# Optimization experiments

Measured on AMD Instinct MI355X. Metric: run time of the kernel, lower is better.

## Reference

```python
import jax, jax.numpy as jnp
import numpy as np


def setup_inputs() -> dict:
    key = jax.random.key(0)
    kq, kk = jax.random.split(key)
    B, Q, K, D = 32, 512, 512, 1024
    queries = jax.random.normal(kq, (B, Q, D), dtype=jnp.float32)
    keys = jax.random.normal(kk, (B, K, D), dtype=jnp.float32)
    # ProbabilityConverter learned scalars (is_temperature=True, is_bias=True)
    temperature = jnp.ones((), dtype=jnp.float32)
    bias = jnp.zeros((), dtype=jnp.float32)
    return {"queries": queries, "keys": keys, "temperature": temperature, "bias": bias}


def reference(queries, keys, temperature, bias):
    # Dot scoring: (B, Q, D) x (B, K, D) -> (B, Q, K)
    logits = jnp.einsum("bqd,bkd->bqk", queries, keys)
    # keys.eq(0.0)[:, :, :1].transpose(1, 2): mask positions where first key feature == 0
    key_mask = (keys[:, :, 0] == 0.0)[:, None, :]  # (B, 1, K)
    neg_inf = jnp.array(-jnp.inf, dtype=logits.dtype)
    logits = jnp.where(key_mask, neg_inf, logits)
    # confidence = sigmoid((logsumexp(logits) + bias) * temperature)
    approx_max_logit = jax.nn.logsumexp(logits, axis=-1)  # (B, Q)
    confidence = jax.nn.sigmoid((approx_max_logit + bias) * temperature)
    attn = jax.nn.softmax(logits, axis=-1)  # (B, Q, K)
    return attn, confidence
```

## Files before the change

kernel.cpp:

```cpp
#include <hip/hip_runtime.h>
#include <math.h>
#include <stdint.h>


#define NB 32
#define NQ 512
#define NK 512
#define ND 1024
#define BK 32
#define NT (ND / BK)
#define BM1 64
#define BM5 64
#define ASTRIDE 520
#define TILE_BYTES 65536
#define WS_TILES ((size_t)NB * NT * TILE_BYTES)
#define WS_TOTAL (WS_TILES + (size_t)NB * NK * 4)

typedef __attribute__((ext_vector_type(8))) short short8;
typedef __attribute__((ext_vector_type(4))) float f32x4;

__device__ __forceinline__ void bf_split(float x, unsigned& hbits, float& lo) {
  unsigned u = __float_as_uint(x);
  unsigned r = u + 0x7fffu + ((u >> 16) & 1u);
  hbits = r & 0xffff0000u;
  lo = x - __uint_as_float(hbits);
}
__device__ __forceinline__ unsigned pack_rn(float x0, float x1) {
  unsigned u0 = __float_as_uint(x0), u1 = __float_as_uint(x1);
  unsigned r0 = u0 + 0x7fffu + ((u0 >> 16) & 1u);
  unsigned r1 = u1 + 0x7fffu + ((u1 >> 16) & 1u);
  return (r0 >> 16) | (r1 & 0xffff0000u);
}

__device__ __forceinline__ int lds_off_write(int r, int c4) {
  int slot = ((c4 >> 1) + (r >> 1)) & 3;
  return r * 32 + slot * 8 + (c4 & 1) * 4;
}
__device__ __forceinline__ int lds_off_read(int r, int quad) {
  int slot = (quad + (r >> 1)) & 3;
  return r * 32 + slot * 8;
}

__global__ __launch_bounds__(256)
void convert_k(const float* __restrict__ Kg, unsigned char* __restrict__ ws) {
  const int bx = blockIdx.x;
  const int batch = bx >> 5, kt = bx & 31;
  const float* src = Kg + (size_t)batch * NK * ND + kt * BK;
  unsigned short* hiB = (unsigned short*)(ws + (size_t)bx * TILE_BYTES);
  unsigned short* loB = hiB + 32768 / 2;
  float* maskB = (float*)(ws + WS_TILES) + batch * NK;

#pragma unroll
  for (int i = 0; i < 16; ++i) {
    int idx = threadIdx.x + 256 * i;
    int c = idx >> 3, c4 = idx & 7;
    float4 v = *(const float4*)(src + (size_t)c * ND + c4 * 4);
    unsigned h0, h1, h2, h3;
    float l0, l1, l2, l3;
    bf_split(v.x, h0, l0); bf_split(v.y, h1, l1);
    bf_split(v.z, h2, l2); bf_split(v.w, h3, l3);
    int off = c * 32 + c4 * 4;
    *(uint2*)(&hiB[off]) = make_uint2((h0 >> 16) | h1, (h2 >> 16) | h3);
    *(uint2*)(&loB[off]) = make_uint2(pack_rn(l0, l1), pack_rn(l2, l3));
    if (kt == 0 && c4 == 0) maskB[c] = v.x;
  }
}

#define MFMA_BF16 __builtin_amdgcn_mfma_f32_16x16x32_bf16

#define BODY5(KT, CURB, NXTB)                                                  \
  do {                                                                         \
    if ((KT) + 1 < NT) {                                                       \
      const unsigned char* tb = wsB + (size_t)((KT) + 1) * TILE_BYTES;         \
      _Pragma("unroll") for (int nt = 0; nt < 4; ++nt) {                       \
        NXTB[2 * nt]     = *(const float4*)(tb + nt * 1024 + boff);            \
        NXTB[2 * nt + 1] = *(const float4*)(tb + 32768 + nt * 1024 + boff);    \
      }                                                                        \
    }                                                                          \
    const int ktL = (KT) & 15;                                                 \
    short8 ahi[4], alo[4];                                                     \
    _Pragma("unroll") for (int mt = 0; mt < 4; ++mt) {                         \
      int off = (mt * 16 + ln15) * ASTRIDE + ktL * 32 + quad * 8;              \
      ahi[mt] = *(const short8*)(&sAhi[off]);                                  \
      alo[mt] = *(const short8*)(&sAlo[off]);                                  \
    }                                                                          \
    _Pragma("unroll") for (int nt = 0; nt < 4; ++nt) {                         \
      short8 bhi = *(const short8*)(&CURB[2 * nt]);                            \
      short8 blo = *(const short8*)(&CURB[2 * nt + 1]);                        \
      _Pragma("unroll") for (int mt = 0; mt < 4; ++mt) {                       \
        acc[mt][nt] = MFMA_BF16(ahi[mt], bhi, acc[mt][nt], 0, 0, 0);           \
        acc[mt][nt] = MFMA_BF16(ahi[mt], blo, acc[mt][nt], 0, 0, 0);           \
        acc[mt][nt] = MFMA_BF16(alo[mt], bhi, acc[mt][nt], 0, 0, 0);           \
      }                                                                        \
    }                                                                          \
  } while (0)

__global__ __launch_bounds__(512, 2)
void attn_fused_v5(const float* __restrict__ Qg,
                   const unsigned char* __restrict__ ws,
                   const float* __restrict__ Tp, const float* __restrict__ Bp,
                   float* __restrict__ attn, float* __restrict__ conf) {
  __shared__ __align__(16) unsigned short sAhi[BM5 * ASTRIDE];
  __shared__ __align__(16) unsigned short sAlo[BM5 * ASTRIDE];
  __shared__ __align__(16) float sRedA[BM5][8];
  __shared__ __align__(16) float sRedB[BM5][8];

  const int tid = threadIdx.x;
  const int g = blockIdx.x;
  const int batch = (g & 7) | (((g >> 3) & 3) << 3);
  const int q0 = (g >> 5) * BM5;
  const int ln = tid & 63, w = tid >> 6;
  const int ln15 = ln & 15, quad = ln >> 4;
  const int col0 = w * 64;

  const float* Qp = Qg + ((size_t)batch * NQ + q0) * ND;
  const unsigned char* wsB = ws + (size_t)batch * NT * TILE_BYTES;
  const float* maskB = (const float*)(ws + WS_TILES) + batch * NK;

  const int boff = (col0 << 6) + (ln15 << 6) + (quad << 4);

  f32x4 acc[4][4];
#pragma unroll
  for (int mt = 0; mt < 4; ++mt)
#pragma unroll
    for (int nt = 0; nt < 4; ++nt) acc[mt][nt] = (f32x4){0.f, 0.f, 0.f, 0.f};

  auto stage_half = [&](int h) {
#pragma unroll
    for (int i = 0; i < 16; ++i) {
      int idx = tid + 512 * i;
      int row = idx >> 7, kc4 = idx & 127;
      float4 v = *(const float4*)(Qp + (size_t)row * ND + h * 512 + kc4 * 4);
      unsigned h0, h1, h2, h3;
      float l0, l1, l2, l3;
      bf_split(v.x, h0, l0); bf_split(v.y, h1, l1);
      bf_split(v.z, h2, l2); bf_split(v.w, h3, l3);
      int off = row * ASTRIDE + kc4 * 4;
      *(uint2*)(&sAhi[off]) = make_uint2((h0 >> 16) | h1, (h2 >> 16) | h3);
      *(uint2*)(&sAlo[off]) = make_uint2(pack_rn(l0, l1), pack_rn(l2, l3));
    }
  };

  stage_half(0);
  float4 pbA[8], pbB[8];
#pragma unroll
  for (int nt = 0; nt < 4; ++nt) {
    pbA[2 * nt]     = *(const float4*)(wsB + nt * 1024 + boff);
    pbA[2 * nt + 1] = *(const float4*)(wsB + 32768 + nt * 1024 + boff);
  }
  __syncthreads();

#pragma unroll 1
  for (int kt = 0; kt < 16; kt += 2) {
    BODY5(kt, pbA, pbB);
    BODY5(kt + 1, pbB, pbA);
  }

  __syncthreads();
  stage_half(1);
  __syncthreads();

#pragma unroll 1
  for (int kt = 16; kt < 32; kt += 2) {
    BODY5(kt, pbA, pbB);
    BODY5(kt + 1, pbB, pbA);
  }

  const float NEGINF = -__builtin_inff();
  float rm[4][4];
#pragma unroll
  for (int mt = 0; mt < 4; ++mt)
#pragma unroll
    for (int rg = 0; rg < 4; ++rg) rm[mt][rg] = NEGINF;

#pragma unroll
  for (int nt = 0; nt < 4; ++nt) {
    int col = col0 + nt * 16 + ln15;
    bool msk = (maskB[col] == 0.0f);
#pragma unroll
    for (int mt = 0; mt < 4; ++mt)
#pragma unroll
      for (int rg = 0; rg < 4; ++rg) {
        float v = msk ? NEGINF : acc[mt][nt][rg];
        acc[mt][nt][rg] = v;
        rm[mt][rg] = fmaxf(rm[mt][rg], v);
      }
  }
#pragma unroll
  for (int mt = 0; mt < 4; ++mt)
#pragma unroll
    for (int rg = 0; rg < 4; ++rg) {
      float v = rm[mt][rg];
#pragma unroll
      for (int d = 1; d < 16; d <<= 1) v = fmaxf(v, __shfl_xor(v, d, 64));
      rm[mt][rg] = v;
    }
  if (ln15 == 0) {
#pragma unroll
    for (int mt = 0; mt < 4; ++mt)
#pragma unroll
      for (int rg = 0; rg < 4; ++rg)
        sRedA[mt * 16 + quad * 4 + rg][w] = rm[mt][rg];
  }
  __syncthreads();

  float gmax[4][4], gsum[4][4];
#pragma unroll
  for (int mt = 0; mt < 4; ++mt)
#pragma unroll
    for (int rg = 0; rg < 4; ++rg) {
      int row = mt * 16 + quad * 4 + rg;
      f32x4 p0 = *(const f32x4*)(&sRedA[row][0]);
      f32x4 p1 = *(const f32x4*)(&sRedA[row][4]);
      gmax[mt][rg] = fmaxf(fmaxf(fmaxf(p0[0], p0[1]), fmaxf(p0[2], p0[3])),
                           fmaxf(fmaxf(p1[0], p1[1]), fmaxf(p1[2], p1[3])));
      gsum[mt][rg] = 0.f;
    }

#pragma unroll
  for (int nt = 0; nt < 4; ++nt)
#pragma unroll
    for (int mt = 0; mt < 4; ++mt)
#pragma unroll
      for (int rg = 0; rg < 4; ++rg) {
        float e = __expf(acc[mt][nt][rg] - gmax[mt][rg]);
        acc[mt][nt][rg] = e;
        gsum[mt][rg] += e;
      }
#pragma unroll
  for (int mt = 0; mt < 4; ++mt)
#pragma unroll
    for (int rg = 0; rg < 4; ++rg) {
      float v = gsum[mt][rg];
#pragma unroll
      for (int d = 1; d < 16; d <<= 1) v += __shfl_xor(v, d, 64);
      gsum[mt][rg] = v;
    }
  if (ln15 == 0) {
#pragma unroll
    for (int mt = 0; mt < 4; ++mt)
#pragma unroll
      for (int rg = 0; rg < 4; ++rg)
        sRedB[mt * 16 + quad * 4 + rg][w] = gsum[mt][rg];
  }
  __syncthreads();
#pragma unroll
  for (int mt = 0; mt < 4; ++mt)
#pragma unroll
    for (int rg = 0; rg < 4; ++rg) {
      int row = mt * 16 + quad * 4 + rg;
      f32x4 p0 = *(const f32x4*)(&sRedB[row][0]);
      f32x4 p1 = *(const f32x4*)(&sRedB[row][4]);
      gsum[mt][rg] = (p0[0] + p0[1]) + (p0[2] + p0[3]) +
                     ((p1[0] + p1[1]) + (p1[2] + p1[3]));
    }

  float* outBase = attn + ((size_t)batch * NQ + q0) * NK;
#pragma unroll
  for (int mt = 0; mt < 4; ++mt)
#pragma unroll
    for (int rg = 0; rg < 4; ++rg) {
      int row = mt * 16 + quad * 4 + rg;
      float inv = 1.0f / gsum[mt][rg];
#pragma unroll
      for (int nt = 0; nt < 4; ++nt)
        outBase[(size_t)row * NK + col0 + nt * 16 + ln15] = acc[mt][nt][rg] * inv;
    }

  if (w == 0 && ln15 == 0) {
    float tv = Tp[0], bv = Bp[0];
#pragma unroll
    for (int mt = 0; mt < 4; ++mt)
#pragma unroll
      for (int rg = 0; rg < 4; ++rg) {
        int row = mt * 16 + quad * 4 + rg;
        float lse = gmax[mt][rg] + __logf(gsum[mt][rg]);
        float t = (lse + bv) * tv;
        conf[(size_t)batch * NQ + q0 + row] = 1.0f / (1.0f + __expf(-t));
      }
  }
}

__global__ __launch_bounds__(256, 1)
void attn_fused_v1(const float* __restrict__ Qg, const float* __restrict__ Kg,
                   const float* __restrict__ Tp, const float* __restrict__ Bp,
                   float* __restrict__ attn, float* __restrict__ conf) {
  __shared__ __align__(16) unsigned short sAhi[BM1 * BK];
  __shared__ __align__(16) unsigned short sAlo[BM1 * BK];
  __shared__ __align__(16) unsigned short sBhi[NK * BK];
  __shared__ __align__(16) unsigned short sBlo[NK * BK];
  __shared__ float sRedA[4][BM1];
  __shared__ float sRedB[4][BM1];

  const int tid = threadIdx.x;
  const int g = blockIdx.x;
  const int batch = (g & 7) | (((g >> 3) & 3) << 3);
  const int q0 = (g >> 5) * BM1;
  const int ln = tid & 63, w = tid >> 6;
  const int ln15 = ln & 15, quad = ln >> 4;
  const int wn0 = w * 128;

  const float* Qp = Qg + ((size_t)batch * NQ + q0) * ND;
  const float* Kp = Kg + (size_t)batch * NK * ND;

  f32x4 acc[4][8];
#pragma unroll
  for (int mt = 0; mt < 4; ++mt)
#pragma unroll
    for (int nt = 0; nt < 8; ++nt) acc[mt][nt] = (f32x4){0.f, 0.f, 0.f, 0.f};

  float4 pb[16], pa[2];
#pragma unroll
  for (int i = 0; i < 16; ++i) {
    int idx = tid + 256 * i, r = idx >> 3, c4 = idx & 7;
    pb[i] = *(const float4*)(Kp + (size_t)r * ND + c4 * 4);
  }
#pragma unroll
  for (int i = 0; i < 2; ++i) {
    int idx = tid + 256 * i, r = idx >> 3, c4 = idx & 7;
    pa[i] = *(const float4*)(Qp + (size_t)r * ND + c4 * 4);
  }

  for (int kt = 0; kt < NT; ++kt) {
    if (kt) __syncthreads();
#pragma unroll
    for (int i = 0; i < 2; ++i) {
      int idx = tid + 256 * i, r = idx >> 3, c4 = idx & 7;
      int off = lds_off_write(r, c4);
      unsigned h0, h1, h2, h3; float l0, l1, l2, l3;
      bf_split(pa[i].x, h0, l0); bf_split(pa[i].y, h1, l1);
      bf_split(pa[i].z, h2, l2); bf_split(pa[i].w, h3, l3);
      *(uint2*)(&sAhi[off]) = make_uint2((h0 >> 16) | h1, (h2 >> 16) | h3);
      *(uint2*)(&sAlo[off]) = make_uint2(pack_rn(l0, l1), pack_rn(l2, l3));
    }
#pragma unroll
    for (int i = 0; i < 16; ++i) {
      int idx = tid + 256 * i, r = idx >> 3, c4 = idx & 7;
      int off = lds_off_write(r, c4);
      unsigned h0, h1, h2, h3; float l0, l1, l2, l3;
      bf_split(pb[i].x, h0, l0); bf_split(pb[i].y, h1, l1);
      bf_split(pb[i].z, h2, l2); bf_split(pb[i].w, h3, l3);
      *(uint2*)(&sBhi[off]) = make_uint2((h0 >> 16) | h1, (h2 >> 16) | h3);
      *(uint2*)(&sBlo[off]) = make_uint2(pack_rn(l0, l1), pack_rn(l2, l3));
    }
    __syncthreads();

    if (kt < NT - 1) {
      const float* Kq = Kp + (kt + 1) * BK;
      const float* Qq = Qp + (kt + 1) * BK;
#pragma unroll
      for (int i = 0; i < 16; ++i) {
        int idx = tid + 256 * i, r = idx >> 3, c4 = idx & 7;
        pb[i] = *(const float4*)(Kq + (size_t)r * ND + c4 * 4);
      }
#pragma unroll
      for (int i = 0; i < 2; ++i) {
        int idx = tid + 256 * i, r = idx >> 3, c4 = idx & 7;
        pa[i] = *(const float4*)(Qq + (size_t)r * ND + c4 * 4);
      }
    }

    short8 ahi[4], alo[4];
#pragma unroll
    for (int mt = 0; mt < 4; ++mt) {
      int off = lds_off_read(mt * 16 + ln15, quad);
      ahi[mt] = *(const short8*)(&sAhi[off]);
      alo[mt] = *(const short8*)(&sAlo[off]);
    }
#pragma unroll
    for (int nt = 0; nt < 8; ++nt) {
      int off = lds_off_read(wn0 + nt * 16 + ln15, quad);
      short8 bhi = *(const short8*)(&sBhi[off]);
      short8 blo = *(const short8*)(&sBlo[off]);
#pragma unroll
      for (int mt = 0; mt < 4; ++mt) {
        acc[mt][nt] = MFMA_BF16(ahi[mt], bhi, acc[mt][nt], 0, 0, 0);
        acc[mt][nt] = MFMA_BF16(ahi[mt], blo, acc[mt][nt], 0, 0, 0);
        acc[mt][nt] = MFMA_BF16(alo[mt], bhi, acc[mt][nt], 0, 0, 0);
      }
    }
  }

  const float NEGINF = -__builtin_inff();
  float rm[4][4];
#pragma unroll
  for (int mt = 0; mt < 4; ++mt)
#pragma unroll
    for (int rg = 0; rg < 4; ++rg) rm[mt][rg] = NEGINF;
#pragma unroll
  for (int nt = 0; nt < 8; ++nt) {
    int col = wn0 + nt * 16 + ln15;
    bool msk = (Kp[(size_t)col * ND] == 0.0f);
#pragma unroll
    for (int mt = 0; mt < 4; ++mt)
#pragma unroll
      for (int rg = 0; rg < 4; ++rg) {
        float v = msk ? NEGINF : acc[mt][nt][rg];
        acc[mt][nt][rg] = v;
        rm[mt][rg] = fmaxf(rm[mt][rg], v);
      }
  }
#pragma unroll
  for (int mt = 0; mt < 4; ++mt)
#pragma unroll
    for (int rg = 0; rg < 4; ++rg) {
      float v = rm[mt][rg];
#pragma unroll
      for (int d = 1; d < 16; d <<= 1) v = fmaxf(v, __shfl_xor(v, d, 64));
      rm[mt][rg] = v;
    }
  if (ln15 == 0)
#pragma unroll
    for (int mt = 0; mt < 4; ++mt)
#pragma unroll
      for (int rg = 0; rg < 4; ++rg)
        sRedA[w][mt * 16 + quad * 4 + rg] = rm[mt][rg];
  __syncthreads();

  float gmax[4][4], gsum[4][4];
#pragma unroll
  for (int mt = 0; mt < 4; ++mt)
#pragma unroll
    for (int rg = 0; rg < 4; ++rg) {
      int row = mt * 16 + quad * 4 + rg;
      gmax[mt][rg] = fmaxf(fmaxf(sRedA[0][row], sRedA[1][row]),
                           fmaxf(sRedA[2][row], sRedA[3][row]));
      gsum[mt][rg] = 0.f;
    }
#pragma unroll
  for (int nt = 0; nt < 8; ++nt)
#pragma unroll
    for (int mt = 0; mt < 4; ++mt)
#pragma unroll
      for (int rg = 0; rg < 4; ++rg) {
        float e = __expf(acc[mt][nt][rg] - gmax[mt][rg]);
        acc[mt][nt][rg] = e;
        gsum[mt][rg] += e;
      }
#pragma unroll
  for (int mt = 0; mt < 4; ++mt)
#pragma unroll
    for (int rg = 0; rg < 4; ++rg) {
      float v = gsum[mt][rg];
#pragma unroll
      for (int d = 1; d < 16; d <<= 1) v += __shfl_xor(v, d, 64);
      gsum[mt][rg] = v;
    }
  if (ln15 == 0)
#pragma unroll
    for (int mt = 0; mt < 4; ++mt)
#pragma unroll
      for (int rg = 0; rg < 4; ++rg)
        sRedB[w][mt * 16 + quad * 4 + rg] = gsum[mt][rg];
  __syncthreads();
#pragma unroll
  for (int mt = 0; mt < 4; ++mt)
#pragma unroll
    for (int rg = 0; rg < 4; ++rg) {
      int row = mt * 16 + quad * 4 + rg;
      gsum[mt][rg] = sRedB[0][row] + sRedB[1][row] + sRedB[2][row] + sRedB[3][row];
    }

  float* outBase = attn + ((size_t)batch * NQ + q0) * NK;
#pragma unroll
  for (int mt = 0; mt < 4; ++mt)
#pragma unroll
    for (int rg = 0; rg < 4; ++rg) {
      int row = mt * 16 + quad * 4 + rg;
      float inv = 1.0f / gsum[mt][rg];
#pragma unroll
      for (int nt = 0; nt < 8; ++nt)
        outBase[(size_t)row * NK + wn0 + nt * 16 + ln15] = acc[mt][nt][rg] * inv;
    }
  if (w == 0 && ln15 == 0) {
    float tv = Tp[0], bv = Bp[0];
#pragma unroll
    for (int mt = 0; mt < 4; ++mt)
#pragma unroll
      for (int rg = 0; rg < 4; ++rg) {
        int row = mt * 16 + quad * 4 + rg;
        float lse = gmax[mt][rg] + __logf(gsum[mt][rg]);
        float t = (lse + bv) * tv;
        conf[(size_t)batch * NQ + q0 + row] = 1.0f / (1.0f + __expf(-t));
      }
  }
}

extern "C" void kernel_launch(void* const* d_in, const int* in_sizes, int n_in,
                              void* d_out, int out_size, void* d_ws, size_t ws_size,
                              hipStream_t stream) {
  const float* q = (const float*)d_in[0];
  const float* k = (const float*)d_in[1];
  const float* temp = (const float*)d_in[2];
  const float* bias = (const float*)d_in[3];
  float* attn = (float*)d_out;
  float* conf = attn + (size_t)NB * NQ * NK;

  if (ws_size >= WS_TOTAL) {
    hipLaunchKernelGGL(convert_k, dim3(NB * NT), dim3(256), 0, stream,
                       k, (unsigned char*)d_ws);
    hipLaunchKernelGGL(attn_fused_v5, dim3(NB * (NQ / BM5)), dim3(512), 0, stream,
                       q, (const unsigned char*)d_ws, temp, bias, attn, conf);
  } else {
    hipLaunchKernelGGL(attn_fused_v1, dim3(NB * (NQ / BM1)), dim3(256), 0, stream,
                       q, k, temp, bias, attn, conf);
  }
}
```

Baseline: 212.6 us.

## Split bf16x3 GEMM into two passes with separate hi/lo key planes

```diff
diff --git a/kernel.cpp b/kernel.cpp
--- a/kernel.cpp
+++ b/kernel.cpp
@@ -10,10 +10,13 @@
 #define BK 32
 #define NT (ND / BK)
 #define BM1 64
-#define BM5 64
-#define ASTRIDE 520
+#define BM6 64
+#define AS1 520
+#define AS2 1032
 #define TILE_BYTES 65536
-#define WS_TILES ((size_t)NB * NT * TILE_BYTES)
+#define PLANE_BYTES (NT * 32768)
+#define BATCH_WS (2 * PLANE_BYTES)
+#define WS_TILES ((size_t)NB * BATCH_WS)
 #define WS_TOTAL (WS_TILES + (size_t)NB * NK * 4)
 
 typedef __attribute__((ext_vector_type(8))) short short8;
@@ -31,6 +34,10 @@
   unsigned r1 = u1 + 0x7fffu + ((u1 >> 16) & 1u);
   return (r0 >> 16) | (r1 & 0xffff0000u);
 }
+__device__ __forceinline__ unsigned hi_rn(float x) {
+  unsigned u = __float_as_uint(x);
+  return (u + 0x7fffu + ((u >> 16) & 1u)) & 0xffff0000u;
+}
 
 __device__ __forceinline__ int lds_off_write(int r, int c4) {
   int slot = ((c4 >> 1) + (r >> 1)) & 3;
@@ -46,8 +53,9 @@
   const int bx = blockIdx.x;
   const int batch = bx >> 5, kt = bx & 31;
   const float* src = Kg + (size_t)batch * NK * ND + kt * BK;
-  unsigned short* hiB = (unsigned short*)(ws + (size_t)bx * TILE_BYTES);
-  unsigned short* loB = hiB + 32768 / 2;
+  unsigned short* hiB =
+      (unsigned short*)(ws + (size_t)batch * BATCH_WS + (size_t)kt * 32768);
+  unsigned short* loB = (unsigned short*)((unsigned char*)hiB + PLANE_BYTES);
   float* maskB = (float*)(ws + WS_TILES) + batch * NK;
 
 #pragma unroll
@@ -68,53 +76,71 @@
 
 #define MFMA_BF16 __builtin_amdgcn_mfma_f32_16x16x32_bf16
 
-#define BODY5(KT, CURB, NXTB)                                                  \
+#define BODY_P1(KT, CURB, NXTB)                                                \
   do {                                                                         \
     if ((KT) + 1 < NT) {                                                       \
-      const unsigned char* tb = wsB + (size_t)((KT) + 1) * TILE_BYTES;         \
-      _Pragma("unroll") for (int nt = 0; nt < 4; ++nt) {                       \
-        NXTB[2 * nt]     = *(const float4*)(tb + nt * 1024 + boff);            \
-        NXTB[2 * nt + 1] = *(const float4*)(tb + 32768 + nt * 1024 + boff);    \
-      }                                                                        \
+      const unsigned char* tb = wsHi + (size_t)((KT) + 1) * 32768;             \
+      _Pragma("unroll") for (int nt = 0; nt < 4; ++nt)                         \
+        NXTB[nt] = *(const f32x4*)(tb + nt * 1024 + boff);                     \
     }                                                                          \
     const int ktL = (KT) & 15;                                                 \
     short8 ahi[4], alo[4];                                                     \
     _Pragma("unroll") for (int mt = 0; mt < 4; ++mt) {                         \
-      int off = (mt * 16 + ln15) * ASTRIDE + ktL * 32 + quad * 8;              \
+      int off = (mt * 16 + ln15) * AS1 + ktL * 32 + quad * 8;                  \
       ahi[mt] = *(const short8*)(&sAhi[off]);                                  \
       alo[mt] = *(const short8*)(&sAlo[off]);                                  \
     }                                                                          \
     _Pragma("unroll") for (int nt = 0; nt < 4; ++nt) {                         \
-      short8 bhi = *(const short8*)(&CURB[2 * nt]);                            \
-      short8 blo = *(const short8*)(&CURB[2 * nt + 1]);                        \
+      short8 bhi = *(const short8*)(&CURB[nt]);                                \
       _Pragma("unroll") for (int mt = 0; mt < 4; ++mt) {                       \
         acc[mt][nt] = MFMA_BF16(ahi[mt], bhi, acc[mt][nt], 0, 0, 0);           \
-        acc[mt][nt] = MFMA_BF16(ahi[mt], blo, acc[mt][nt], 0, 0, 0);           \
         acc[mt][nt] = MFMA_BF16(alo[mt], bhi, acc[mt][nt], 0, 0, 0);           \
       }                                                                        \
     }                                                                          \
   } while (0)
 
+#define BODY_P2(KT, CURB, NXTB)                                                \
+  do {                                                                         \
+    if ((KT) + 1 < NT) {                                                       \
+      const unsigned char* tb = wsLo + (size_t)((KT) + 1) * 32768;             \
+      _Pragma("unroll") for (int nt = 0; nt < 4; ++nt)                         \
+        NXTB[nt] = *(const f32x4*)(tb + nt * 1024 + boff);                     \
+    }                                                                          \
+    short8 ahi2[4];                                                            \
+    _Pragma("unroll") for (int mt = 0; mt < 4; ++mt) {                         \
+      int off = (mt * 16 + ln15) * AS2 + (KT) * 32 + quad * 8;                 \
+      ahi2[mt] = *(const short8*)(&sA2[off]);                                  \
+    }                                                                          \
+    _Pragma("unroll") for (int nt = 0; nt < 4; ++nt) {                         \
+      short8 blo = *(const short8*)(&CURB[nt]);                                \
+      _Pragma("unroll") for (int mt = 0; mt < 4; ++mt)                         \
+        acc[mt][nt] = MFMA_BF16(ahi2[mt], blo, acc[mt][nt], 0, 0, 0);          \
+    }                                                                          \
+  } while (0)
+
 __global__ __launch_bounds__(512, 2)
-void attn_fused_v5(const float* __restrict__ Qg,
+void attn_fused_v6(const float* __restrict__ Qg,
                    const unsigned char* __restrict__ ws,
                    const float* __restrict__ Tp, const float* __restrict__ Bp,
                    float* __restrict__ attn, float* __restrict__ conf) {
-  __shared__ __align__(16) unsigned short sAhi[BM5 * ASTRIDE];
-  __shared__ __align__(16) unsigned short sAlo[BM5 * ASTRIDE];
-  __shared__ __align__(16) float sRedA[BM5][8];
-  __shared__ __align__(16) float sRedB[BM5][8];
+  __shared__ __align__(16) unsigned short sU[2 * BM6 * AS1];
+  __shared__ __align__(16) float sRedA[BM6][8];
+  __shared__ __align__(16) float sRedB[BM6][8];
+  unsigned short* sAhi = sU;
+  unsigned short* sAlo = sU + BM6 * AS1;
+  unsigned short* sA2 = sU;
 
   const int tid = threadIdx.x;
   const int g = blockIdx.x;
-  const int batch = (g & 7) | (((g >> 3) & 3) << 3);
-  const int q0 = (g >> 5) * BM5;
+  const int batch = g & 31;
+  const int q0 = (g >> 5) * BM6;
   const int ln = tid & 63, w = tid >> 6;
   const int ln15 = ln & 15, quad = ln >> 4;
   const int col0 = w * 64;
 
   const float* Qp = Qg + ((size_t)batch * NQ + q0) * ND;
-  const unsigned char* wsB = ws + (size_t)batch * NT * TILE_BYTES;
+  const unsigned char* wsHi = ws + (size_t)batch * BATCH_WS;
+  const unsigned char* wsLo = wsHi + PLANE_BYTES;
   const float* maskB = (const float*)(ws + WS_TILES) + batch * NK;
 
   const int boff = (col0 << 6) + (ln15 << 6) + (quad << 4);
@@ -125,45 +151,70 @@
 #pragma unroll
     for (int nt = 0; nt < 4; ++nt) acc[mt][nt] = (f32x4){0.f, 0.f, 0.f, 0.f};
 
-  auto stage_half = [&](int h) {
+  auto stage_p1 = [&](int h) {
 #pragma unroll
     for (int i = 0; i < 16; ++i) {
       int idx = tid + 512 * i;
       int row = idx >> 7, kc4 = idx & 127;
-      float4 v = *(const float4*)(Qp + (size_t)row * ND + h * 512 + kc4 * 4);
+      f32x4 v = __builtin_nontemporal_load(
+          (const f32x4*)(Qp + (size_t)row * ND + h * 512 + kc4 * 4));
       unsigned h0, h1, h2, h3;
       float l0, l1, l2, l3;
-      bf_split(v.x, h0, l0); bf_split(v.y, h1, l1);
-      bf_split(v.z, h2, l2); bf_split(v.w, h3, l3);
-      int off = row * ASTRIDE + kc4 * 4;
+      bf_split(v[0], h0, l0); bf_split(v[1], h1, l1);
+      bf_split(v[2], h2, l2); bf_split(v[3], h3, l3);
+      int off = row * AS1 + kc4 * 4;
       *(uint2*)(&sAhi[off]) = make_uint2((h0 >> 16) | h1, (h2 >> 16) | h3);
       *(uint2*)(&sAlo[off]) = make_uint2(pack_rn(l0, l1), pack_rn(l2, l3));
     }
   };
-
-  stage_half(0);
-  float4 pbA[8], pbB[8];
-#pragma unroll
-  for (int nt = 0; nt < 4; ++nt) {
-    pbA[2 * nt]     = *(const float4*)(wsB + nt * 1024 + boff);
-    pbA[2 * nt + 1] = *(const float4*)(wsB + 32768 + nt * 1024 + boff);
-  }
+  auto stage_p2 = [&]() {
+#pragma unroll
+    for (int i = 0; i < 32; ++i) {
+      int idx = tid + 512 * i;
+      int row = idx >> 8, kc4 = idx & 255;
+      f32x4 v = __builtin_nontemporal_load(
+          (const f32x4*)(Qp + (size_t)row * ND + kc4 * 4));
+      unsigned h0 = hi_rn(v[0]), h1 = hi_rn(v[1]);
+      unsigned h2 = hi_rn(v[2]), h3 = hi_rn(v[3]);
+      int off = row * AS2 + kc4 * 4;
+      *(uint2*)(&sA2[off]) = make_uint2((h0 >> 16) | h1, (h2 >> 16) | h3);
+    }
+  };
+
+  float4 pbA_[4], pbB_[4];
+  f32x4* pbA = (f32x4*)pbA_;
+  f32x4* pbB = (f32x4*)pbB_;
+
+  stage_p1(0);
+#pragma unroll
+  for (int nt = 0; nt < 4; ++nt)
+    pbA[nt] = *(const f32x4*)(wsHi + nt * 1024 + boff);
   __syncthreads();
 
 #pragma unroll 1
   for (int kt = 0; kt < 16; kt += 2) {
-    BODY5(kt, pbA, pbB);
-    BODY5(kt + 1, pbB, pbA);
-  }
-
-  __syncthreads();
-  stage_half(1);
-  __syncthreads();
-
+    BODY_P1(kt, pbA, pbB);
+    BODY_P1(kt + 1, pbB, pbA);
+  }
+  __syncthreads();
+  stage_p1(1);
+  __syncthreads();
 #pragma unroll 1
   for (int kt = 16; kt < 32; kt += 2) {
-    BODY5(kt, pbA, pbB);
-    BODY5(kt + 1, pbB, pbA);
+    BODY_P1(kt, pbA, pbB);
+    BODY_P1(kt + 1, pbB, pbA);
+  }
+
+  __syncthreads();
+#pragma unroll
+  for (int nt = 0; nt < 4; ++nt)
+    pbA[nt] = *(const f32x4*)(wsLo + nt * 1024 + boff);
+  stage_p2();
+  __syncthreads();
+#pragma unroll 1
+  for (int kt = 0; kt < 32; kt += 2) {
+    BODY_P2(kt, pbA, pbB);
+    BODY_P2(kt + 1, pbB, pbA);
   }
 
   const float NEGINF = -__builtin_inff();
@@ -264,7 +315,9 @@
       float inv = 1.0f / gsum[mt][rg];
 #pragma unroll
       for (int nt = 0; nt < 4; ++nt)
-        outBase[(size_t)row * NK + col0 + nt * 16 + ln15] = acc[mt][nt][rg] * inv;
+        __builtin_nontemporal_store(
+            acc[mt][nt][rg] * inv,
+            &outBase[(size_t)row * NK + col0 + nt * 16 + ln15]);
     }
 
   if (w == 0 && ln15 == 0) {
@@ -294,7 +347,7 @@
 
   const int tid = threadIdx.x;
   const int g = blockIdx.x;
-  const int batch = (g & 7) | (((g >> 3) & 3) << 3);
+  const int batch = g & 31;
   const int q0 = (g >> 5) * BM1;
   const int ln = tid & 63, w = tid >> 6;
   const int ln15 = ln & 15, quad = ln >> 4;
@@ -499,7 +552,7 @@
   if (ws_size >= WS_TOTAL) {
     hipLaunchKernelGGL(convert_k, dim3(NB * NT), dim3(256), 0, stream,
                        k, (unsigned char*)d_ws);
-    hipLaunchKernelGGL(attn_fused_v5, dim3(NB * (NQ / BM5)), dim3(512), 0, stream,
+    hipLaunchKernelGGL(attn_fused_v6, dim3(NB * (NQ / BM6)), dim3(512), 0, stream,
                        q, (const unsigned char*)d_ws, temp, bias, attn, conf);
   } else {
     hipLaunchKernelGGL(attn_fused_v1, dim3(NB * (NQ / BM1)), dim3(256), 0, stream,
```

Result: slower. 223.8 us (+5.3%).

## Double block width to 1024 threads with 16 waves each owning 32 key columns

Applied to the files above, without the earlier changes.

```diff
diff --git a/kernel.cpp b/kernel.cpp
--- a/kernel.cpp
+++ b/kernel.cpp
@@ -10,7 +10,7 @@
 #define BK 32
 #define NT (ND / BK)
 #define BM1 64
-#define BM5 64
+#define BM7 64
 #define ASTRIDE 520
 #define TILE_BYTES 65536
 #define WS_TILES ((size_t)NB * NT * TILE_BYTES)
@@ -68,14 +68,14 @@
 
 #define MFMA_BF16 __builtin_amdgcn_mfma_f32_16x16x32_bf16
 
-#define BODY5(KT, CURB, NXTB)                                                  \
+#define BODY7(KT, CURB, NXTB)                                                  \
   do {                                                                         \
     if ((KT) + 1 < NT) {                                                       \
       const unsigned char* tb = wsB + (size_t)((KT) + 1) * TILE_BYTES;         \
-      _Pragma("unroll") for (int nt = 0; nt < 4; ++nt) {                       \
-        NXTB[2 * nt]     = *(const float4*)(tb + nt * 1024 + boff);            \
-        NXTB[2 * nt + 1] = *(const float4*)(tb + 32768 + nt * 1024 + boff);    \
-      }                                                                        \
+      NXTB[0] = *(const f32x4*)(tb + boff);                                    \
+      NXTB[1] = *(const f32x4*)(tb + 1024 + boff);                             \
+      NXTB[2] = *(const f32x4*)(tb + 32768 + boff);                            \
+      NXTB[3] = *(const f32x4*)(tb + 32768 + 1024 + boff);                     \
     }                                                                          \
     const int ktL = (KT) & 15;                                                 \
     short8 ahi[4], alo[4];                                                     \
@@ -84,9 +84,9 @@
       ahi[mt] = *(const short8*)(&sAhi[off]);                                  \
       alo[mt] = *(const short8*)(&sAlo[off]);                                  \
     }                                                                          \
-    _Pragma("unroll") for (int nt = 0; nt < 4; ++nt) {                         \
-      short8 bhi = *(const short8*)(&CURB[2 * nt]);                            \
-      short8 blo = *(const short8*)(&CURB[2 * nt + 1]);                        \
+    _Pragma("unroll") for (int nt = 0; nt < 2; ++nt) {                         \
+      short8 bhi = *(const short8*)(&CURB[nt]);                                \
+      short8 blo = *(const short8*)(&CURB[2 + nt]);                            \
       _Pragma("unroll") for (int mt = 0; mt < 4; ++mt) {                       \
         acc[mt][nt] = MFMA_BF16(ahi[mt], bhi, acc[mt][nt], 0, 0, 0);           \
         acc[mt][nt] = MFMA_BF16(ahi[mt], blo, acc[mt][nt], 0, 0, 0);           \
@@ -95,23 +95,23 @@
     }                                                                          \
   } while (0)
 
-__global__ __launch_bounds__(512, 2)
-void attn_fused_v5(const float* __restrict__ Qg,
+__global__ __launch_bounds__(1024, 4)
+void attn_fused_v7(const float* __restrict__ Qg,
                    const unsigned char* __restrict__ ws,
                    const float* __restrict__ Tp, const float* __restrict__ Bp,
                    float* __restrict__ attn, float* __restrict__ conf) {
-  __shared__ __align__(16) unsigned short sAhi[BM5 * ASTRIDE];
-  __shared__ __align__(16) unsigned short sAlo[BM5 * ASTRIDE];
-  __shared__ __align__(16) float sRedA[BM5][8];
-  __shared__ __align__(16) float sRedB[BM5][8];
+  __shared__ __align__(16) unsigned short sAhi[BM7 * ASTRIDE];
+  __shared__ __align__(16) unsigned short sAlo[BM7 * ASTRIDE];
+  __shared__ __align__(16) float sRedA[BM7][16];
+  __shared__ __align__(16) float sRedB[BM7][16];
 
   const int tid = threadIdx.x;
   const int g = blockIdx.x;
-  const int batch = (g & 7) | (((g >> 3) & 3) << 3);
-  const int q0 = (g >> 5) * BM5;
+  const int batch = g & 31;
+  const int q0 = (g >> 5) * BM7;
   const int ln = tid & 63, w = tid >> 6;
   const int ln15 = ln & 15, quad = ln >> 4;
-  const int col0 = w * 64;
+  const int col0 = w * 32;
 
   const float* Qp = Qg + ((size_t)batch * NQ + q0) * ND;
   const unsigned char* wsB = ws + (size_t)batch * NT * TILE_BYTES;
@@ -119,41 +119,48 @@
 
   const int boff = (col0 << 6) + (ln15 << 6) + (quad << 4);
 
-  f32x4 acc[4][4];
-#pragma unroll
-  for (int mt = 0; mt < 4; ++mt)
-#pragma unroll
-    for (int nt = 0; nt < 4; ++nt) acc[mt][nt] = (f32x4){0.f, 0.f, 0.f, 0.f};
+  f32x4 acc[4][2];
+#pragma unroll
+  for (int mt = 0; mt < 4; ++mt)
+#pragma unroll
+    for (int nt = 0; nt < 2; ++nt) acc[mt][nt] = (f32x4){0.f, 0.f, 0.f, 0.f};
 
   auto stage_half = [&](int h) {
 #pragma unroll
-    for (int i = 0; i < 16; ++i) {
-      int idx = tid + 512 * i;
-      int row = idx >> 7, kc4 = idx & 127;
-      float4 v = *(const float4*)(Qp + (size_t)row * ND + h * 512 + kc4 * 4);
-      unsigned h0, h1, h2, h3;
-      float l0, l1, l2, l3;
-      bf_split(v.x, h0, l0); bf_split(v.y, h1, l1);
-      bf_split(v.z, h2, l2); bf_split(v.w, h3, l3);
-      int off = row * ASTRIDE + kc4 * 4;
-      *(uint2*)(&sAhi[off]) = make_uint2((h0 >> 16) | h1, (h2 >> 16) | h3);
-      *(uint2*)(&sAlo[off]) = make_uint2(pack_rn(l0, l1), pack_rn(l2, l3));
+    for (int i = 0; i < 4; ++i) {
+      int idx = tid + 1024 * i;
+      int row = idx >> 6, kc8 = idx & 63;
+      const float* p = Qp + (size_t)row * ND + h * 512 + kc8 * 8;
+      float4 va = *(const float4*)(p);
+      float4 vb = *(const float4*)(p + 4);
+      unsigned h0, h1, h2, h3, h4, h5, h6, h7;
+      float l0, l1, l2, l3, l4, l5, l6, l7;
+      bf_split(va.x, h0, l0); bf_split(va.y, h1, l1);
+      bf_split(va.z, h2, l2); bf_split(va.w, h3, l3);
+      bf_split(vb.x, h4, l4); bf_split(vb.y, h5, l5);
+      bf_split(vb.z, h6, l6); bf_split(vb.w, h7, l7);
+      int off = row * ASTRIDE + kc8 * 8;
+      *(uint4*)(&sAhi[off]) = make_uint4((h0 >> 16) | h1, (h2 >> 16) | h3,
+                                         (h4 >> 16) | h5, (h6 >> 16) | h7);
+      *(uint4*)(&sAlo[off]) = make_uint4(pack_rn(l0, l1), pack_rn(l2, l3),
+                                         pack_rn(l4, l5), pack_rn(l6, l7));
     }
   };
 
   stage_half(0);
-  float4 pbA[8], pbB[8];
-#pragma unroll
-  for (int nt = 0; nt < 4; ++nt) {
-    pbA[2 * nt]     = *(const float4*)(wsB + nt * 1024 + boff);
-    pbA[2 * nt + 1] = *(const float4*)(wsB + 32768 + nt * 1024 + boff);
-  }
+  float4 pbA_[4], pbB_[4];
+  f32x4* pbA = (f32x4*)pbA_;
+  f32x4* pbB = (f32x4*)pbB_;
+  pbA[0] = *(const f32x4*)(wsB + boff);
+  pbA[1] = *(const f32x4*)(wsB + 1024 + boff);
+  pbA[2] = *(const f32x4*)(wsB + 32768 + boff);
+  pbA[3] = *(const f32x4*)(wsB + 32768 + 1024 + boff);
   __syncthreads();
 
 #pragma unroll 1
   for (int kt = 0; kt < 16; kt += 2) {
-    BODY5(kt, pbA, pbB);
-    BODY5(kt + 1, pbB, pbA);
+    BODY7(kt, pbA, pbB);
+    BODY7(kt + 1, pbB, pbA);
   }
 
   __syncthreads();
@@ -162,8 +169,8 @@
 
 #pragma unroll 1
   for (int kt = 16; kt < 32; kt += 2) {
-    BODY5(kt, pbA, pbB);
-    BODY5(kt + 1, pbB, pbA);
+    BODY7(kt, pbA, pbB);
+    BODY7(kt + 1, pbB, pbA);
   }
 
   const float NEGINF = -__builtin_inff();
@@ -174,7 +181,7 @@
     for (int rg = 0; rg < 4; ++rg) rm[mt][rg] = NEGINF;
 
 #pragma unroll
-  for (int nt = 0; nt < 4; ++nt) {
+  for (int nt = 0; nt < 2; ++nt) {
     int col = col0 + nt * 16 + ln15;
     bool msk = (maskB[col] == 0.0f);
 #pragma unroll
@@ -212,13 +219,18 @@
       int row = mt * 16 + quad * 4 + rg;
       f32x4 p0 = *(const f32x4*)(&sRedA[row][0]);
       f32x4 p1 = *(const f32x4*)(&sRedA[row][4]);
-      gmax[mt][rg] = fmaxf(fmaxf(fmaxf(p0[0], p0[1]), fmaxf(p0[2], p0[3])),
-                           fmaxf(fmaxf(p1[0], p1[1]), fmaxf(p1[2], p1[3])));
+      f32x4 p2 = *(const f32x4*)(&sRedA[row][8]);
+      f32x4 p3 = *(const f32x4*)(&sRedA[row][12]);
+      float m01 = fmaxf(fmaxf(fmaxf(p0[0], p0[1]), fmaxf(p0[2], p0[3])),
+                        fmaxf(fmaxf(p1[0], p1[1]), fmaxf(p1[2], p1[3])));
+      float m23 = fmaxf(fmaxf(fmaxf(p2[0], p2[1]), fmaxf(p2[2], p2[3])),
+                        fmaxf(fmaxf(p3[0], p3[1]), fmaxf(p3[2], p3[3])));
+      gmax[mt][rg] = fmaxf(m01, m23);
       gsum[mt][rg] = 0.f;
     }
 
 #pragma unroll
-  for (int nt = 0; nt < 4; ++nt)
+  for (int nt = 0; nt < 2; ++nt)
 #pragma unroll
     for (int mt = 0; mt < 4; ++mt)
 #pragma unroll
@@ -251,8 +263,12 @@
       int row = mt * 16 + quad * 4 + rg;
       f32x4 p0 = *(const f32x4*)(&sRedB[row][0]);
       f32x4 p1 = *(const f32x4*)(&sRedB[row][4]);
-      gsum[mt][rg] = (p0[0] + p0[1]) + (p0[2] + p0[3]) +
-                     ((p1[0] + p1[1]) + (p1[2] + p1[3]));
+      f32x4 p2 = *(const f32x4*)(&sRedB[row][8]);
+      f32x4 p3 = *(const f32x4*)(&sRedB[row][12]);
+      gsum[mt][rg] = ((p0[0] + p0[1]) + (p0[2] + p0[3])) +
+                     ((p1[0] + p1[1]) + (p1[2] + p1[3])) +
+                     ((p2[0] + p2[1]) + (p2[2] + p2[3])) +
+                     ((p3[0] + p3[1]) + (p3[2] + p3[3]));
     }
 
   float* outBase = attn + ((size_t)batch * NQ + q0) * NK;
@@ -263,7 +279,7 @@
       int row = mt * 16 + quad * 4 + rg;
       float inv = 1.0f / gsum[mt][rg];
 #pragma unroll
-      for (int nt = 0; nt < 4; ++nt)
+      for (int nt = 0; nt < 2; ++nt)
         outBase[(size_t)row * NK + col0 + nt * 16 + ln15] = acc[mt][nt][rg] * inv;
     }
 
@@ -294,7 +310,7 @@
 
   const int tid = threadIdx.x;
   const int g = blockIdx.x;
-  const int batch = (g & 7) | (((g >> 3) & 3) << 3);
+  const int batch = g & 31;
   const int q0 = (g >> 5) * BM1;
   const int ln = tid & 63, w = tid >> 6;
   const int ln15 = ln & 15, quad = ln >> 4;
@@ -499,7 +515,7 @@
   if (ws_size >= WS_TOTAL) {
     hipLaunchKernelGGL(convert_k, dim3(NB * NT), dim3(256), 0, stream,
                        k, (unsigned char*)d_ws);
-    hipLaunchKernelGGL(attn_fused_v5, dim3(NB * (NQ / BM5)), dim3(512), 0, stream,
+    hipLaunchKernelGGL(attn_fused_v7, dim3(NB * (NQ / BM7)), dim3(1024), 0, stream,
                        q, (const unsigned char*)d_ws, temp, bias, attn, conf);
   } else {
     hipLaunchKernelGGL(attn_fused_v1, dim3(NB * (NQ / BM1)), dim3(256), 0, stream,
```

Result: slower. 218.0 us (+2.5%).
